# Kernel optimization log

Measured on AMD Instinct MI355X. Metric: run time of the kernel, lower is better.

## Reference

```python
import jax, jax.numpy as jnp
import numpy as np

HIDDEN = 1024
NUM_EXPERTS = 16
TOP_K = 6
EPS = 1e-10


def setup_inputs() -> dict:
    key = jax.random.key(0)
    k1, k2, k3, k4 = jax.random.split(key, 4)
    tokens = jax.random.normal(k1, (4, 2048, HIDDEN), dtype=jnp.float32)
    # torch.nn.Linear(hidden_size, num_experts): weight [E, H], bias [E]
    bound = 1.0 / np.sqrt(HIDDEN)
    router_w = jax.random.uniform(k2, (NUM_EXPERTS, HIDDEN), jnp.float32, -bound, bound)
    router_b = jax.random.uniform(k3, (NUM_EXPERTS,), jnp.float32, -bound, bound)
    # expert_weights = randn(E, H, H) / sqrt(H)
    expert_w = jax.random.normal(k4, (NUM_EXPERTS, HIDDEN, HIDDEN), dtype=jnp.float32) / np.sqrt(HIDDEN)
    return {"tokens": tokens, "router_w": router_w, "router_b": router_b, "expert_w": expert_w}


def reference(tokens, router_w, router_b, expert_w):
    B, S, H = tokens.shape
    E = expert_w.shape[0]
    T = B * S

    # Router: softmax -> top-k -> renormalize top-k probs
    logits = jnp.einsum("bsh,eh->bse", tokens, router_w) + router_b  # [B,S,E]
    probs = jax.nn.softmax(logits, axis=-1)
    top_p, top_i = jax.lax.top_k(probs, TOP_K)                        # [B,S,K]
    top_p = top_p / (jnp.sum(top_p, axis=-1, keepdims=True) + EPS)

    x = tokens.reshape(T, H)
    flat_i = top_i.reshape(T, TOP_K)
    flat_p = top_p.reshape(T, TOP_K)

    # Dense gate matrix [T, E]: scatter of normalized top-k weights.
    # Equivalent to the expand/sort/pad + weighted scatter-add restore.
    gate = jnp.zeros((T, E), dtype=flat_p.dtype)
    gate = gate.at[jnp.arange(T)[:, None], flat_i].add(flat_p)
    acc = jnp.maximum(jnp.sum(gate, axis=-1), EPS)  # weight accumulator (clamp min=1e-10)

    # Grouped GEMM equivalent: per-expert matmul weighted by gate, accumulated.
    out = jnp.zeros_like(x)
    for e in range(E):  # fixed, small structural loop over experts
        out = out + (x @ expert_w[e]) * gate[:, e:e + 1]
    out = (out / acc[:, None]).reshape(B, S, H)

    # 'dummy' gradient-connection term from restore_output_with_triton_and_gradients
    out = out + EPS * jnp.sum(top_p, axis=-1, keepdims=True)
    return out
```

## Files before the change

kernel.cpp:

```cpp
#include <hip/hip_runtime.h>
#include <cstdint>
#include <cstddef>

#define NE 16
#define TOPK 6
#define HID 1024
#define NTOK 8192
#define EPSF 1e-10f
#define CAP_ROWS 51200
#define MAXB256 208
#define NT 16

typedef short bf16x8 __attribute__((ext_vector_type(8)));
typedef float f32x4 __attribute__((ext_vector_type(4)));

__device__ __forceinline__ unsigned int f2bf_rne(float f) {
  union { float f; unsigned int u; } v;
  v.f = f;
  return (v.u + 0x7FFFu + ((v.u >> 16) & 1u)) >> 16;
}

__device__ __forceinline__ float bfbits2f(unsigned int hi16) {
  union { unsigned int u; float f; } v;
  v.u = hi16 << 16;
  return v.f;
}

__device__ __forceinline__ void load_lds16(const void* g, void* l) {
  __builtin_amdgcn_global_load_lds(
      (const __attribute__((address_space(1))) void*)g,
      (__attribute__((address_space(3))) void*)l, 16, 0, 0);
}

__global__ __launch_bounds__(256) void router_sparse_kernel(
    const float* __restrict__ tokens, const float* __restrict__ rw,
    const float* __restrict__ rb, unsigned short* __restrict__ Xb,
    unsigned int* __restrict__ topk, float* __restrict__ g6,
    float* __restrict__ epst) {
  __shared__ float s_rw[NE * HID];
  const int tid = threadIdx.x;
  const int wv = tid >> 6;
  const int lane = tid & 63;
  const int token = blockIdx.x * 4 + wv;

  for (int i = tid; i < NE * HID / 4; i += 256)
    ((float4*)s_rw)[i] = ((const float4*)rw)[i];
  __syncthreads();

  const float* xp = tokens + (size_t)token * HID;
  float x[16];
#pragma unroll
  for (int j = 0; j < 16; ++j) x[j] = xp[lane + 64 * j];

  unsigned short* xbrow = Xb + (size_t)token * HID;
#pragma unroll
  for (int j = 0; j < 16; ++j)
    xbrow[lane + 64 * j] = (unsigned short)f2bf_rne(x[j]);

  float lg[NE];
#pragma unroll
  for (int e = 0; e < NE; ++e) {
    const float* w = s_rw + e * HID;
    float p = 0.f;
#pragma unroll
    for (int j = 0; j < 16; ++j) p += x[j] * w[lane + 64 * j];
    lg[e] = p;
  }
#pragma unroll
  for (int m = 1; m < 64; m <<= 1) {
#pragma unroll
    for (int e = 0; e < NE; ++e) lg[e] += __shfl_xor(lg[e], m);
  }
  float mx = -1e30f;
#pragma unroll
  for (int e = 0; e < NE; ++e) {
    lg[e] += rb[e];
    mx = fmaxf(mx, lg[e]);
  }
  float q[NE];
  float s_all = 0.f;
#pragma unroll
  for (int e = 0; e < NE; ++e) {
    q[e] = expf(lg[e] - mx);
    s_all += q[e];
  }
  unsigned sel = 0, pack = 0;
  float s_top = 0.f;
  float gq[TOPK];
#pragma unroll
  for (int k = 0; k < TOPK; ++k) {
    float best = -1.f;
    int bi = 0;
#pragma unroll
    for (int e = 0; e < NE; ++e) {
      bool taken = (sel >> e) & 1u;
      if (!taken && q[e] > best) { best = q[e]; bi = e; }
    }
    sel |= 1u << bi;
    gq[k] = best;
    s_top += best;
    pack |= ((unsigned)bi) << (4 * k);
  }
  if (lane < TOPK)
    g6[(size_t)token * TOPK + lane] = gq[lane] / s_top;
  if (lane == 32) {
    topk[token] = pack;
    float s = s_top / s_all;
    epst[token] = EPSF * (s / (s + EPSF));
  }
}

__global__ __launch_bounds__(256) void prep_kernel(
    const float* __restrict__ ew, unsigned short* __restrict__ wt,
    const unsigned int* __restrict__ topk, const float* __restrict__ g6,
    unsigned int* __restrict__ tokmap, float* __restrict__ gpos,
    unsigned int* __restrict__ inv, unsigned int* __restrict__ table,
    unsigned int* __restrict__ total) {
  __shared__ float tile[64][65];
  __shared__ unsigned int hist[NE];
  __shared__ unsigned int s_seg[NE];
  __shared__ unsigned int s_sc[256];
  const int tid = threadIdx.x;

  if (blockIdx.x >= NE) {
    const int q = blockIdx.x - NE;
    const int e2 = q >> 8;
    const int ntile = ((q >> 4) & 15) * 64;
    const int ktile = (q & 15) * 64;
    const int tr = tid >> 6;
    const int tc = tid & 63;
    const float* wp = ew + (size_t)e2 * HID * HID;
#pragma unroll
    for (int r = 0; r < 64; r += 4)
      tile[r + tr][tc] = wp[(size_t)(ktile + r + tr) * HID + ntile + tc];
    __syncthreads();
    unsigned short* wo = wt + (size_t)e2 * HID * HID;
    const int aa = tid & 31;
    const int rg = tid >> 5;
#pragma unroll
    for (int c2 = 0; c2 < 64; c2 += 8) {
      const int n = c2 + rg;
      const unsigned lo = f2bf_rne(tile[2 * aa][n]);
      const unsigned hi = f2bf_rne(tile[2 * aa + 1][n]);
      *(unsigned int*)(wo + (size_t)(ntile + n) * HID + ktile + 2 * aa) =
          lo | (hi << 16);
    }
    return;
  }

  const int e = blockIdx.x;

  if (tid < NE) hist[tid] = 0;
  __syncthreads();
  for (int t = tid; t < NTOK; t += 256) {
    const unsigned p = topk[t];
#pragma unroll
    for (int k = 0; k < TOPK; ++k) atomicAdd(&hist[(p >> (4 * k)) & 15u], 1u);
  }
  __syncthreads();
  if (tid == 0) {
    unsigned off = 0;
    for (int i = 0; i < NE; ++i) {
      s_seg[i] = off;
      off += ((hist[i] + 127) >> 7) << 7;
    }
  }
  __syncthreads();
  if (e == 0 && tid == 0) {
    unsigned b = 0;
    for (int i = 0; i < NE; ++i) {
      const unsigned nb = (hist[i] + 127) >> 7;
      const unsigned seg = s_seg[i];
      unsigned m = 0;
      for (; m + 2 <= nb; m += 2)
        table[b++] = ((unsigned)i << 24) | (seg + m * 128);
      if (m < nb)
        table[b++] = ((unsigned)i << 24) | (1u << 23) | (seg + m * 128);
    }
    *total = b;
  }

  const int tbase = tid * (NTOK / 256);
  unsigned c = 0;
  for (int i = 0; i < NTOK / 256; ++i) {
    const unsigned p = topk[tbase + i];
#pragma unroll
    for (int k = 0; k < TOPK; ++k) c += (((p >> (4 * k)) & 15u) == (unsigned)e);
  }
  s_sc[tid] = c;
  __syncthreads();
  for (int off = 1; off < 256; off <<= 1) {
    unsigned v = (tid >= off) ? s_sc[tid - off] : 0u;
    __syncthreads();
    s_sc[tid] += v;
    __syncthreads();
  }
  const unsigned seg0 = s_seg[e];
  unsigned pos = seg0 + s_sc[tid] - c;
  for (int i = 0; i < NTOK / 256; ++i) {
    const int t = tbase + i;
    const unsigned p = topk[t];
#pragma unroll
    for (int k = 0; k < TOPK; ++k) {
      if (((p >> (4 * k)) & 15u) == (unsigned)e) {
        tokmap[pos] = (unsigned)t;
        gpos[pos] = g6[(size_t)t * TOPK + k];
        inv[(size_t)t * TOPK + k] = pos;
        ++pos;
      }
    }
  }
  const unsigned cnt_e = s_sc[255];
  const unsigned segend = seg0 + (((cnt_e + 127) >> 7) << 7);
  for (unsigned p2 = seg0 + cnt_e + tid; p2 < segend; p2 += 256) {
    tokmap[p2] = 0u;
    gpos[p2] = 0.f;
  }
}

__global__ __launch_bounds__(512, 2) void moe_ggemm_kernel(
    const unsigned short* __restrict__ Xb, const unsigned short* __restrict__ Wt,
    const unsigned int* __restrict__ table, const unsigned int* __restrict__ total,
    const unsigned int* __restrict__ tokmap, const float* __restrict__ gpos,
    unsigned short* __restrict__ Y) {
  __shared__ unsigned short As[2][256][64];
  __shared__ unsigned short Bs[2][256][64];
  __shared__ unsigned int Ts[256];
  __shared__ float Gs[256];

  const unsigned tot = *total;
  const unsigned bx = blockIdx.x;
  const unsigned wg = (bx & 7u) * (MAXB256 * 4u / 8u) + (bx >> 3);
  const unsigned slot = wg >> 2;
  if (slot >= tot) return;
  const int n0 = (int)(wg & 3u) * 256;
  const unsigned ent = table[slot];
  const int e = (int)(ent >> 24);
  const int half = (int)((ent >> 23) & 1u);
  const int row0 = (int)(ent & 0x7FFFFFu);

  const int tid = threadIdx.x;
  const int wv = tid >> 6;
  const int lane = tid & 63;
  const int lm = lane & 15;
  const int quad = lane >> 4;
  const int wvm = wv >> 2;
  const int woff_m = wvm * 128;
  const int woff_n = (wv & 3) * 64;

  if (tid < 256) {
    const int rc = (half && tid >= 128) ? 127 : tid;
    Ts[tid] = tokmap[row0 + rc];
    Gs[tid] = (half && tid >= 128) ? 0.f : gpos[row0 + rc];
  }
  __syncthreads();

  const int srow = tid >> 3;
  const int scol = ((tid & 7) ^ (srow & 7)) << 4;
  const char* pA[4];
  const char* pB[4];
#pragma unroll
  for (int i = 0; i < 4; ++i) {
    pA[i] = (const char*)Xb + (size_t)Ts[i * 64 + srow] * (HID * 2) + scol;
    pB[i] = (const char*)Wt + (size_t)e * (HID * HID * 2) +
            (size_t)(n0 + i * 64 + srow) * (HID * 2) + scol;
  }
  char* const Ab = (char*)&As[0][0][0];
  char* const Bb = (char*)&Bs[0][0][0];
  const int sdst = wv * 8 * 128;

  load_lds16(pA[0], Ab + 0 * 8192 + sdst);
  load_lds16(pA[2], Ab + 2 * 8192 + sdst);
  load_lds16(pB[0], Bb + 0 * 8192 + sdst);
  load_lds16(pB[1], Bb + 1 * 8192 + sdst);
  load_lds16(pB[2], Bb + 2 * 8192 + sdst);
  load_lds16(pB[3], Bb + 3 * 8192 + sdst);
  load_lds16(pA[1], Ab + 1 * 8192 + sdst);
  load_lds16(pA[3], Ab + 3 * 8192 + sdst);

  f32x4 acc[8][4];
#pragma unroll
  for (int f = 0; f < 8; ++f)
#pragma unroll
    for (int g = 0; g < 4; ++g) acc[f][g] = (f32x4){0.f, 0.f, 0.f, 0.f};

  const int rsw = (lm & 7) << 4;
  const int roff0 = (quad * 16) ^ rsw;
  const int roff1 = (64 + quad * 16) ^ rsw;

  asm volatile("s_waitcnt vmcnt(2)" ::: "memory");
  __builtin_amdgcn_s_barrier();

  for (int kt = 0; kt < NT; ++kt) {
    const int c = kt & 1;
    const int koff = (kt < NT - 1 ? kt + 1 : kt) * 128;
    const char* ab = Ab + c * 32768;
    const char* bb = Bb + c * 32768;
    char* const ast = Ab + (c ^ 1) * 32768;
    char* const bst = Bb + (c ^ 1) * 32768;

    bf16x8 a[4][2], b[4][2];

#pragma unroll
    for (int f = 0; f < 4; ++f) {
      const char* rp = ab + (woff_m + 16 * f + lm) * 128;
      a[f][0] = *(const bf16x8*)(rp + roff0);
      a[f][1] = *(const bf16x8*)(rp + roff1);
    }
#pragma unroll
    for (int g = 0; g < 2; ++g) {
      const char* rp = bb + (woff_n + 16 * g + lm) * 128;
      b[g][0] = *(const bf16x8*)(rp + roff0);
      b[g][1] = *(const bf16x8*)(rp + roff1);
    }
    load_lds16(pA[0] + koff, ast + 0 * 8192 + sdst);
    load_lds16(pA[2] + koff, ast + 2 * 8192 + sdst);
    __builtin_amdgcn_s_barrier();
    asm volatile("s_waitcnt lgkmcnt(0)" ::: "memory");
    __builtin_amdgcn_s_setprio(1);
#pragma unroll
    for (int f = 0; f < 4; ++f)
#pragma unroll
      for (int g = 0; g < 2; ++g) {
        acc[f][g] = __builtin_amdgcn_mfma_f32_16x16x32_bf16(a[f][0], b[g][0], acc[f][g], 0, 0, 0);
        acc[f][g] = __builtin_amdgcn_mfma_f32_16x16x32_bf16(a[f][1], b[g][1], acc[f][g], 0, 0, 0);
      }
    __builtin_amdgcn_s_setprio(0);
    __builtin_amdgcn_s_barrier();

#pragma unroll
    for (int g = 2; g < 4; ++g) {
      const char* rp = bb + (woff_n + 16 * g + lm) * 128;
      b[g][0] = *(const bf16x8*)(rp + roff0);
      b[g][1] = *(const bf16x8*)(rp + roff1);
    }
    load_lds16(pB[0] + koff, bst + 0 * 8192 + sdst);
    load_lds16(pB[1] + koff, bst + 1 * 8192 + sdst);
    __builtin_amdgcn_s_barrier();
    asm volatile("s_waitcnt lgkmcnt(0)" ::: "memory");
    __builtin_amdgcn_s_setprio(1);
#pragma unroll
    for (int f = 0; f < 4; ++f)
#pragma unroll
      for (int g = 2; g < 4; ++g) {
        acc[f][g] = __builtin_amdgcn_mfma_f32_16x16x32_bf16(a[f][0], b[g][0], acc[f][g], 0, 0, 0);
        acc[f][g] = __builtin_amdgcn_mfma_f32_16x16x32_bf16(a[f][1], b[g][1], acc[f][g], 0, 0, 0);
      }
    __builtin_amdgcn_s_setprio(0);
    asm volatile("s_waitcnt vmcnt(4)" ::: "memory");
    __builtin_amdgcn_s_barrier();

#pragma unroll
    for (int f = 0; f < 4; ++f) {
      const char* rp = ab + (woff_m + 16 * (f + 4) + lm) * 128;
      a[f][0] = *(const bf16x8*)(rp + roff0);
      a[f][1] = *(const bf16x8*)(rp + roff1);
    }
    load_lds16(pB[2] + koff, bst + 2 * 8192 + sdst);
    load_lds16(pB[3] + koff, bst + 3 * 8192 + sdst);
    __builtin_amdgcn_s_barrier();
    asm volatile("s_waitcnt lgkmcnt(0)" ::: "memory");
    __builtin_amdgcn_s_setprio(1);
#pragma unroll
    for (int f = 0; f < 4; ++f)
#pragma unroll
      for (int g = 2; g < 4; ++g) {
        acc[f + 4][g] = __builtin_amdgcn_mfma_f32_16x16x32_bf16(a[f][0], b[g][0], acc[f + 4][g], 0, 0, 0);
        acc[f + 4][g] = __builtin_amdgcn_mfma_f32_16x16x32_bf16(a[f][1], b[g][1], acc[f + 4][g], 0, 0, 0);
      }
    __builtin_amdgcn_s_setprio(0);
    __builtin_amdgcn_s_barrier();

    load_lds16(pA[1] + koff, ast + 1 * 8192 + sdst);
    load_lds16(pA[3] + koff, ast + 3 * 8192 + sdst);
    __builtin_amdgcn_s_barrier();
    __builtin_amdgcn_s_setprio(1);
#pragma unroll
    for (int f = 0; f < 4; ++f)
#pragma unroll
      for (int g = 0; g < 2; ++g) {
        acc[f + 4][g] = __builtin_amdgcn_mfma_f32_16x16x32_bf16(a[f][0], b[g][0], acc[f + 4][g], 0, 0, 0);
        acc[f + 4][g] = __builtin_amdgcn_mfma_f32_16x16x32_bf16(a[f][1], b[g][1], acc[f + 4][g], 0, 0, 0);
      }
    __builtin_amdgcn_s_setprio(0);
    asm volatile("s_waitcnt vmcnt(2)" ::: "memory");
    __builtin_amdgcn_s_barrier();
  }

  asm volatile("s_waitcnt vmcnt(0)" ::: "memory");

  if (!(half && wvm)) {
#pragma unroll
    for (int f = 0; f < 8; ++f)
#pragma unroll
      for (int r = 0; r < 4; ++r) {
        const int row = woff_m + 16 * f + quad * 4 + r;
        const float gte = Gs[row];
        unsigned short* yrow = Y + (size_t)(row0 + row) * HID + n0;
#pragma unroll
        for (int g = 0; g < 4; ++g)
          yrow[woff_n + 16 * g + lm] = (unsigned short)f2bf_rne(gte * acc[f][g][r]);
      }
  }
}

__global__ __launch_bounds__(256) void reduce_kernel(
    const unsigned short* __restrict__ Y, const unsigned int* __restrict__ inv,
    const float* __restrict__ epst, float* __restrict__ out) {
  const int sub = threadIdx.x >> 7;
  const int ct = threadIdx.x & 127;
  const int t = blockIdx.x * 2 + sub;
  const int c0 = ct * 8;

  float s[8];
  const float ep = epst[t];
#pragma unroll
  for (int i = 0; i < 8; ++i) s[i] = ep;

#pragma unroll
  for (int k = 0; k < TOPK; ++k) {
    const unsigned pos = inv[(size_t)t * TOPK + k];
    const uint4 v = *(const uint4*)(Y + (size_t)pos * HID + c0);
    s[0] += bfbits2f(v.x & 0xFFFFu);
    s[1] += bfbits2f(v.x >> 16);
    s[2] += bfbits2f(v.y & 0xFFFFu);
    s[3] += bfbits2f(v.y >> 16);
    s[4] += bfbits2f(v.z & 0xFFFFu);
    s[5] += bfbits2f(v.z >> 16);
    s[6] += bfbits2f(v.w & 0xFFFFu);
    s[7] += bfbits2f(v.w >> 16);
  }
  float* orow = out + (size_t)t * HID + c0;
  *(float4*)orow = (float4){s[0], s[1], s[2], s[3]};
  *(float4*)(orow + 4) = (float4){s[4], s[5], s[6], s[7]};
}

extern "C" void kernel_launch(void* const* d_in, const int* in_sizes, int n_in,
                              void* d_out, int out_size, void* d_ws, size_t ws_size,
                              hipStream_t stream) {
  const float* tokens = (const float*)d_in[0];
  const float* rw = (const float*)d_in[1];
  const float* rb = (const float*)d_in[2];
  const float* ew = (const float*)d_in[3];
  float* out = (float*)d_out;

  char* ws = (char*)d_ws;
  const size_t OFF_XB = 0;
  const size_t OFF_WT = 16777216;
  const size_t OFF_Y = 50331648;
  const size_t OFF_META = 155189248;
  const size_t M_TOKMAP = OFF_META + 0;
  const size_t M_GPOS = OFF_META + 204800;
  const size_t M_TOTAL = OFF_META + 409600;
  const size_t M_TABLE = OFF_META + 409664;
  const size_t M_INV = OFF_META + 411328;
  const size_t M_TOPK = OFF_META + 607936;
  const size_t M_G6 = OFF_META + 640704;
  const size_t M_EPST = OFF_META + 837312;

  unsigned short* Xb = (unsigned short*)(ws + OFF_XB);
  unsigned short* Wt = (unsigned short*)(ws + OFF_WT);
  unsigned short* Y = (unsigned short*)(ws + OFF_Y);
  unsigned int* tokmap = (unsigned int*)(ws + M_TOKMAP);
  float* gpos = (float*)(ws + M_GPOS);
  unsigned int* total = (unsigned int*)(ws + M_TOTAL);
  unsigned int* table = (unsigned int*)(ws + M_TABLE);
  unsigned int* inv = (unsigned int*)(ws + M_INV);
  unsigned int* topk = (unsigned int*)(ws + M_TOPK);
  float* g6 = (float*)(ws + M_G6);
  float* epst = (float*)(ws + M_EPST);

  router_sparse_kernel<<<dim3(NTOK / 4), dim3(256), 0, stream>>>(
      tokens, rw, rb, Xb, topk, g6, epst);
  prep_kernel<<<dim3(NE + (HID / 64) * (HID / 64) * NE), dim3(256), 0, stream>>>(
      ew, Wt, topk, g6, tokmap, gpos, inv, table, total);
  moe_ggemm_kernel<<<dim3(MAXB256 * 4), dim3(512), 0, stream>>>(
      Xb, Wt, table, total, tokmap, gpos, Y);
  reduce_kernel<<<dim3(NTOK / 2), dim3(256), 0, stream>>>(Y, inv, epst, out);
}
```

Before: 364.6 us.

## Fuse weight transpose into router kernel and split sort-assign into lean kernel

Moves the expert-weight bf16 transpose blocks into the router kernel's grid, so routing and weight conversion share one launch. The sort/assign step runs as its own 16-block, 1024-thread kernel that builds the histogram with a shared-memory reduction instead of atomics. The router now reads tokens and router weights as float4 straight from global memory instead of staging 64KB of weights in LDS, which frees LDS and raises occupancy. Xb is written as packed bf16 pairs. The risk is more global-memory reads of the router weights, which are likely served from cache.

```diff
diff --git a/kernel.cpp b/kernel.cpp
--- a/kernel.cpp
+++ b/kernel.cpp
@@ -10,6 +10,7 @@
 #define CAP_ROWS 51200
 #define MAXB256 208
 #define NT 16
+#define ROUTER_BLKS 2048
 
 typedef short bf16x8 __attribute__((ext_vector_type(8)));
 typedef float f32x4 __attribute__((ext_vector_type(4)));
@@ -32,38 +33,69 @@
       (__attribute__((address_space(3))) void*)l, 16, 0, 0);
 }
 
-__global__ __launch_bounds__(256) void router_sparse_kernel(
+__global__ __launch_bounds__(256) void fused_pre_kernel(
     const float* __restrict__ tokens, const float* __restrict__ rw,
     const float* __restrict__ rb, unsigned short* __restrict__ Xb,
     unsigned int* __restrict__ topk, float* __restrict__ g6,
-    float* __restrict__ epst) {
-  __shared__ float s_rw[NE * HID];
+    float* __restrict__ epst, const float* __restrict__ ew,
+    unsigned short* __restrict__ wt) {
+  __shared__ float tile[64][65];
   const int tid = threadIdx.x;
+  const unsigned bx = blockIdx.x;
+
+  if (bx >= ROUTER_BLKS) {
+    const int q = bx - ROUTER_BLKS;
+    const int e2 = q >> 8;
+    const int ntile = ((q >> 4) & 15) * 64;
+    const int ktile = (q & 15) * 64;
+    const int tr = tid >> 6;
+    const int tc = tid & 63;
+    const float* wp = ew + (size_t)e2 * HID * HID;
+#pragma unroll
+    for (int r = 0; r < 64; r += 4)
+      tile[r + tr][tc] = wp[(size_t)(ktile + r + tr) * HID + ntile + tc];
+    __syncthreads();
+    unsigned short* wo = wt + (size_t)e2 * HID * HID;
+    const int aa = tid & 31;
+    const int rg = tid >> 5;
+#pragma unroll
+    for (int c2 = 0; c2 < 64; c2 += 8) {
+      const int n = c2 + rg;
+      const unsigned lo = f2bf_rne(tile[2 * aa][n]);
+      const unsigned hi = f2bf_rne(tile[2 * aa + 1][n]);
+      *(unsigned int*)(wo + (size_t)(ntile + n) * HID + ktile + 2 * aa) =
+          lo | (hi << 16);
+    }
+    return;
+  }
+
   const int wv = tid >> 6;
   const int lane = tid & 63;
-  const int token = blockIdx.x * 4 + wv;
-
-  for (int i = tid; i < NE * HID / 4; i += 256)
-    ((float4*)s_rw)[i] = ((const float4*)rw)[i];
-  __syncthreads();
-
-  const float* xp = tokens + (size_t)token * HID;
-  float x[16];
-#pragma unroll
-  for (int j = 0; j < 16; ++j) x[j] = xp[lane + 64 * j];
+  const int token = (int)bx * 4 + wv;
+
+  const float4* xp4 = (const float4*)(tokens + (size_t)token * HID);
+  float4 x4[4];
+#pragma unroll
+  for (int j = 0; j < 4; ++j) x4[j] = xp4[lane + 64 * j];
 
   unsigned short* xbrow = Xb + (size_t)token * HID;
 #pragma unroll
-  for (int j = 0; j < 16; ++j)
-    xbrow[lane + 64 * j] = (unsigned short)f2bf_rne(x[j]);
+  for (int j = 0; j < 4; ++j) {
+    const unsigned lo = f2bf_rne(x4[j].x) | (f2bf_rne(x4[j].y) << 16);
+    const unsigned hi = f2bf_rne(x4[j].z) | (f2bf_rne(x4[j].w) << 16);
+    *(uint2*)(xbrow + 4 * (lane + 64 * j)) = (uint2){lo, hi};
+  }
 
   float lg[NE];
 #pragma unroll
   for (int e = 0; e < NE; ++e) {
-    const float* w = s_rw + e * HID;
+    const float4* wp4 = (const float4*)(rw + e * HID);
     float p = 0.f;
 #pragma unroll
-    for (int j = 0; j < 16; ++j) p += x[j] * w[lane + 64 * j];
+    for (int j = 0; j < 4; ++j) {
+      const float4 w = wp4[lane + 64 * j];
+      p += x4[j].x * w.x + x4[j].y * w.y + x4[j].z * w.z + x4[j].w * w.w;
+    }
     lg[e] = p;
   }
 #pragma unroll
@@ -110,52 +142,35 @@
   }
 }
 
-__global__ __launch_bounds__(256) void prep_kernel(
-    const float* __restrict__ ew, unsigned short* __restrict__ wt,
+__global__ __launch_bounds__(1024) void sortassign_kernel(
     const unsigned int* __restrict__ topk, const float* __restrict__ g6,
     unsigned int* __restrict__ tokmap, float* __restrict__ gpos,
     unsigned int* __restrict__ inv, unsigned int* __restrict__ table,
     unsigned int* __restrict__ total) {
-  __shared__ float tile[64][65];
+  __shared__ unsigned int sred[NE][65];
+  __shared__ unsigned int s_seg[NE];
   __shared__ unsigned int hist[NE];
-  __shared__ unsigned int s_seg[NE];
-  __shared__ unsigned int s_sc[256];
+  __shared__ unsigned int s_sc[1024];
+  const int e = blockIdx.x;
   const int tid = threadIdx.x;
 
-  if (blockIdx.x >= NE) {
-    const int q = blockIdx.x - NE;
-    const int e2 = q >> 8;
-    const int ntile = ((q >> 4) & 15) * 64;
-    const int ktile = (q & 15) * 64;
-    const int tr = tid >> 6;
-    const int tc = tid & 63;
-    const float* wp = ew + (size_t)e2 * HID * HID;
-#pragma unroll
-    for (int r = 0; r < 64; r += 4)
-      tile[r + tr][tc] = wp[(size_t)(ktile + r + tr) * HID + ntile + tc];
-    __syncthreads();
-    unsigned short* wo = wt + (size_t)e2 * HID * HID;
-    const int aa = tid & 31;
-    const int rg = tid >> 5;
-#pragma unroll
-    for (int c2 = 0; c2 < 64; c2 += 8) {
-      const int n = c2 + rg;
-      const unsigned lo = f2bf_rne(tile[2 * aa][n]);
-      const unsigned hi = f2bf_rne(tile[2 * aa + 1][n]);
-      *(unsigned int*)(wo + (size_t)(ntile + n) * HID + ktile + 2 * aa) =
-          lo | (hi << 16);
-    }
-    return;
-  }
-
-  const int e = blockIdx.x;
-
-  if (tid < NE) hist[tid] = 0;
+  {
+    const unsigned hx = tid & 15u;
+    const int hc = tid >> 4;
+    const unsigned int* tp = topk + hc * 128;
+    unsigned hcnt = 0;
+    for (int i = 0; i < 128; ++i) {
+      const unsigned p = tp[i];
+#pragma unroll
+      for (int k = 0; k < TOPK; ++k) hcnt += (((p >> (4 * k)) & 15u) == hx);
+    }
+    sred[hx][hc] = hcnt;
+  }
   __syncthreads();
-  for (int t = tid; t < NTOK; t += 256) {
-    const unsigned p = topk[t];
-#pragma unroll
-    for (int k = 0; k < TOPK; ++k) atomicAdd(&hist[(p >> (4 * k)) & 15u], 1u);
+  if (tid < NE) {
+    unsigned s = 0;
+    for (int j = 0; j < 64; ++j) s += sred[tid][j];
+    hist[tid] = s;
   }
   __syncthreads();
   if (tid == 0) {
@@ -180,16 +195,16 @@
     *total = b;
   }
 
-  const int tbase = tid * (NTOK / 256);
+  const int tbase = tid * (NTOK / 1024);
   unsigned c = 0;
-  for (int i = 0; i < NTOK / 256; ++i) {
+  for (int i = 0; i < NTOK / 1024; ++i) {
     const unsigned p = topk[tbase + i];
 #pragma unroll
     for (int k = 0; k < TOPK; ++k) c += (((p >> (4 * k)) & 15u) == (unsigned)e);
   }
   s_sc[tid] = c;
   __syncthreads();
-  for (int off = 1; off < 256; off <<= 1) {
+  for (int off = 1; off < 1024; off <<= 1) {
     unsigned v = (tid >= off) ? s_sc[tid - off] : 0u;
     __syncthreads();
     s_sc[tid] += v;
@@ -197,7 +212,7 @@
   }
   const unsigned seg0 = s_seg[e];
   unsigned pos = seg0 + s_sc[tid] - c;
-  for (int i = 0; i < NTOK / 256; ++i) {
+  for (int i = 0; i < NTOK / 1024; ++i) {
     const int t = tbase + i;
     const unsigned p = topk[t];
 #pragma unroll
@@ -210,9 +225,9 @@
       }
     }
   }
-  const unsigned cnt_e = s_sc[255];
+  const unsigned cnt_e = s_sc[1023];
   const unsigned segend = seg0 + (((cnt_e + 127) >> 7) << 7);
-  for (unsigned p2 = seg0 + cnt_e + tid; p2 < segend; p2 += 256) {
+  for (unsigned p2 = seg0 + cnt_e + tid; p2 < segend; p2 += 1024) {
     tokmap[p2] = 0u;
     gpos[p2] = 0.f;
   }
@@ -470,10 +485,10 @@
   float* g6 = (float*)(ws + M_G6);
   float* epst = (float*)(ws + M_EPST);
 
-  router_sparse_kernel<<<dim3(NTOK / 4), dim3(256), 0, stream>>>(
-      tokens, rw, rb, Xb, topk, g6, epst);
-  prep_kernel<<<dim3(NE + (HID / 64) * (HID / 64) * NE), dim3(256), 0, stream>>>(
-      ew, Wt, topk, g6, tokmap, gpos, inv, table, total);
+  fused_pre_kernel<<<dim3(ROUTER_BLKS + (HID / 64) * (HID / 64) * NE), dim3(256),
+                     0, stream>>>(tokens, rw, rb, Xb, topk, g6, epst, ew, Wt);
+  sortassign_kernel<<<dim3(NE), dim3(1024), 0, stream>>>(
+      topk, g6, tokmap, gpos, inv, table, total);
   moe_ggemm_kernel<<<dim3(MAXB256 * 4), dim3(512), 0, stream>>>(
       Xb, Wt, table, total, tokmap, gpos, Y);
   reduce_kernel<<<dim3(NTOK / 2), dim3(256), 0, stream>>>(Y, inv, epst, out);
```

After: 343.1 us. 1.06x faster.
